# Optimization experiments

Measured on AMD Instinct MI355X. Metric: run time of the kernel, lower is better.

The kernel has to match this reference:

```python
import math
import jax, jax.numpy as jnp
import numpy as np

N = 8192
D_IN = 512
D_E = 512


def setup_inputs() -> dict:
    key = jax.random.key(0)
    k1, k2, k3, k4 = jax.random.split(key, 4)
    x = jax.random.normal(k1, (N, D_IN), dtype=jnp.float32)
    A = jax.random.uniform(k2, (N, N), dtype=jnp.float32)
    # xavier-uniform-ish scaling for the two projection weights
    lim_qkv = math.sqrt(6.0 / (D_IN + 3 * D_E))
    Wqkv = jax.random.uniform(k3, (D_IN, 3 * D_E), dtype=jnp.float32, minval=-lim_qkv, maxval=lim_qkv)
    bqkv = jnp.zeros((3 * D_E,), dtype=jnp.float32)
    lim_o = math.sqrt(6.0 / (D_E + D_E))
    Wo = jax.random.uniform(k4, (D_E, D_E), dtype=jnp.float32, minval=-lim_o, maxval=lim_o)
    bo = jnp.zeros((D_E,), dtype=jnp.float32)
    return {"x": x, "A": A, "Wqkv": Wqkv, "bqkv": bqkv, "Wo": Wo, "bo": bo}


def reference(x, A, Wqkv, bqkv, Wo, bo):
    # qkv projection: [N, 3*D_E]
    qkv = x @ Wqkv + bqkv
    q, k, v = jnp.split(qkv, 3, axis=-1)  # each [N, D_E]
    # graph-adjacency transform of keys
    k = A @ k  # [N, D_E]
    scale = 1.0 / math.sqrt(q.shape[-1])
    attn_logits = (q @ k.T) * scale  # [N, N]
    attention = jax.nn.softmax(attn_logits, axis=-1)
    values = attention @ v  # [N, D_E]
    o = values @ Wo + bo
    return (o, attention)
```

## Files before the change

### kernel.cpp

```cpp
#include <hip/hip_runtime.h>

typedef _Float16 half8 __attribute__((ext_vector_type(8)));
typedef _Float16 half4 __attribute__((ext_vector_type(4)));
typedef float f32x4 __attribute__((ext_vector_type(4)));

__global__ __launch_bounds__(256) void transpose_f32(
    const float* __restrict__ in, int lda,
    float* __restrict__ out, int ldo)
{
  __shared__ float t[32][33];
  const int tx = threadIdx.x & 31, ty = threadIdx.x >> 5;
  const int bc = blockIdx.x * 32, br = blockIdx.y * 32;
#pragma unroll
  for (int i = 0; i < 4; ++i)
    t[ty + 8 * i][tx] = in[(size_t)(br + ty + 8 * i) * lda + bc + tx];
  __syncthreads();
#pragma unroll
  for (int i = 0; i < 4; ++i)
    out[(size_t)(bc + ty + 8 * i) * ldo + br + tx] = t[tx][ty + 8 * i];
}

__global__ __launch_bounds__(256) void transpose_f32_f16(
    const float* __restrict__ in, int lda,
    _Float16* __restrict__ out, int ldo)
{
  __shared__ float t[32][33];
  const int tx = threadIdx.x & 31, ty = threadIdx.x >> 5;
  const int bc = blockIdx.x * 32, br = blockIdx.y * 32;
#pragma unroll
  for (int i = 0; i < 4; ++i)
    t[ty + 8 * i][tx] = in[(size_t)(br + ty + 8 * i) * lda + bc + tx];
  __syncthreads();
#pragma unroll
  for (int i = 0; i < 4; ++i)
    out[(size_t)(bc + ty + 8 * i) * ldo + br + tx] = (_Float16)t[tx][ty + 8 * i];
}

__global__ __launch_bounds__(256) void halfcolsum(
    const float* __restrict__ k0T, float* __restrict__ csum)
{
  const int d = blockIdx.x, tid = threadIdx.x;
  const float4* p = (const float4*)(k0T + (size_t)d * 8192);
  float s = 0.f;
#pragma unroll
  for (int i = 0; i < 8; ++i) {
    float4 v = p[i * 256 + tid];
    s += (v.x + v.y) + (v.z + v.w);
  }
#pragma unroll
  for (int off = 32; off; off >>= 1) s += __shfl_xor(s, off);
  __shared__ float r[4];
  if ((tid & 63) == 0) r[tid >> 6] = s;
  __syncthreads();
  if (tid == 0) csum[d] = 0.5f * ((r[0] + r[1]) + (r[2] + r[3]));
}

template<int ASPL,int BSPL,int BM,int BN,int WAVES_M,int WAVES_N,int THREADS,
         int APART,bool KSPLIT,bool QF16,int MINW>
__global__ __launch_bounds__(THREADS, MINW) void gemm_bt(
    const float* __restrict__ Ag, int lda, size_t a_plane,
    const float* __restrict__ Bg, int ldb,
    float* __restrict__ Cg, int ldc, size_t c_plane,
    const float* __restrict__ bias, int K, float scale,
    _Float16* __restrict__ q16out)
{
  constexpr int BK = 32;
  constexpr int WM = BM / WAVES_M, WN = BN / WAVES_N;
  constexpr int FM = WM / 16, FN = WN / 16;
  constexpr int NCA = (BM * 4) / THREADS;
  constexpr int NCB = (BN * 4) / THREADS;
  static_assert((BM * 4) % THREADS == 0 && (BN * 4) % THREADS == 0, "mismatch");

  __shared__ _Float16 ldsA[2][ASPL][BM][BK];
  __shared__ _Float16 ldsB[2][BSPL][BN][BK];

  const int tid  = threadIdx.x;
  const int lane = tid & 63;
  const int wid  = tid >> 6;
  const int wrow = wid / WAVES_N, wcol = wid % WAVES_N;
  const int l15  = lane & 15, g = lane >> 4;
  const int brow = blockIdx.y * BM;
  const int bcol = blockIdx.x * BN;

  if constexpr (KSPLIT) {
    const int kc = blockIdx.z;
    Ag += (size_t)kc * K;
    Bg += (size_t)kc * K;
    Cg += (size_t)kc * c_plane;
  }

  f32x4 acc[FM][FN];
#pragma unroll
  for (int mi = 0; mi < FM; ++mi)
#pragma unroll
    for (int ni = 0; ni < FN; ++ni)
      acc[mi][ni] = (f32x4){0.f, 0.f, 0.f, 0.f};

  float4 ra[NCA][2], rb[NCB][2];

  auto loadAB = [&](int kt) {
    const int k0 = kt * BK;
#pragma unroll
    for (int i = 0; i < NCA; ++i) {
      int c = tid + THREADS * i;
      int row = c >> 2, ci = c & 3;
      const float* bp = Ag + (size_t)(brow + row) * lda + k0 + ci * 8;
      float4 u0 = ((const float4*)bp)[0];
      float4 u1 = ((const float4*)bp)[1];
#pragma unroll
      for (int p = 1; p < APART; ++p) {
        const float* pp = bp + (size_t)p * a_plane;
        float4 w0 = ((const float4*)pp)[0], w1 = ((const float4*)pp)[1];
        u0.x += w0.x; u0.y += w0.y; u0.z += w0.z; u0.w += w0.w;
        u1.x += w1.x; u1.y += w1.y; u1.z += w1.z; u1.w += w1.w;
      }
      ra[i][0] = u0; ra[i][1] = u1;
    }
#pragma unroll
    for (int i = 0; i < NCB; ++i) {
      int c = tid + THREADS * i;
      int row = c >> 2, ci = c & 3;
      const float4* p = (const float4*)(Bg + (size_t)(bcol + row) * ldb + k0 + ci * 8);
      rb[i][0] = p[0]; rb[i][1] = p[1];
    }
  };

  auto stageLDS = [&](int b) {
#pragma unroll
    for (int i = 0; i < NCA; ++i) {
      int c = tid + THREADS * i;
      int row = c >> 2, ci = c & 3;
      float f[8] = {ra[i][0].x, ra[i][0].y, ra[i][0].z, ra[i][0].w,
                    ra[i][1].x, ra[i][1].y, ra[i][1].z, ra[i][1].w};
      half8 h, l;
#pragma unroll
      for (int j = 0; j < 8; ++j) {
        _Float16 hv = (_Float16)f[j];
        h[j] = hv;
        if (ASPL == 2) l[j] = (_Float16)(f[j] - (float)hv);
      }
      int off = row * BK + ((ci ^ ((row >> 1) & 3)) << 3);
      *(half8*)(&ldsA[b][0][0][0] + off) = h;
      if (ASPL == 2) *(half8*)(&ldsA[b][1][0][0] + off) = l;
    }
#pragma unroll
    for (int i = 0; i < NCB; ++i) {
      int c = tid + THREADS * i;
      int row = c >> 2, ci = c & 3;
      float f[8] = {rb[i][0].x, rb[i][0].y, rb[i][0].z, rb[i][0].w,
                    rb[i][1].x, rb[i][1].y, rb[i][1].z, rb[i][1].w};
      half8 h, l;
#pragma unroll
      for (int j = 0; j < 8; ++j) {
        _Float16 hv = (_Float16)f[j];
        h[j] = hv;
        if (BSPL == 2) l[j] = (_Float16)(f[j] - (float)hv);
      }
      int off = row * BK + ((ci ^ ((row >> 1) & 3)) << 3);
      *(half8*)(&ldsB[b][0][0][0] + off) = h;
      if (BSPL == 2) *(half8*)(&ldsB[b][1][0][0] + off) = l;
    }
  };

  const int nk = K / BK;
  loadAB(0);
  stageLDS(0);
  if (nk > 1) loadAB(1);
  __syncthreads();

  for (int kt = 0; kt < nk; ++kt) {
    const int cur = kt & 1, nxt = cur ^ 1;
    if (kt + 1 < nk) stageLDS(nxt);
    if (kt + 2 < nk) loadAB(kt + 2);

    half8 af[FM][ASPL];
#pragma unroll
    for (int mi = 0; mi < FM; ++mi)
#pragma unroll
      for (int sa = 0; sa < ASPL; ++sa) {
        int row = wrow * WM + mi * 16 + l15;
        af[mi][sa] = *(const half8*)(&ldsA[cur][sa][0][0] + row * BK + ((g ^ ((row >> 1) & 3)) << 3));
      }
#pragma unroll
    for (int ni = 0; ni < FN; ++ni) {
      half8 bf[BSPL];
#pragma unroll
      for (int sb = 0; sb < BSPL; ++sb) {
        int row = wcol * WN + ni * 16 + l15;
        bf[sb] = *(const half8*)(&ldsB[cur][sb][0][0] + row * BK + ((g ^ ((row >> 1) & 3)) << 3));
      }
#pragma unroll
      for (int mi = 0; mi < FM; ++mi)
#pragma unroll
        for (int sa = 0; sa < ASPL; ++sa)
#pragma unroll
          for (int sb = 0; sb < BSPL; ++sb) {
            if (ASPL == 2 && BSPL == 2 && sa == 1 && sb == 1) continue;
            acc[mi][ni] = __builtin_amdgcn_mfma_f32_16x16x32_f16(af[mi][sa], bf[sb], acc[mi][ni], 0, 0, 0);
          }
    }
    __syncthreads();
  }

#pragma unroll
  for (int mi = 0; mi < FM; ++mi)
#pragma unroll
    for (int ni = 0; ni < FN; ++ni) {
      int col = bcol + wcol * WN + ni * 16 + l15;
      float bv = bias ? bias[col] : 0.f;
#pragma unroll
      for (int j = 0; j < 4; ++j) {
        int r = brow + wrow * WM + mi * 16 + g * 4 + j;
        float v = acc[mi][ni][j] * scale + bv;
        Cg[(size_t)r * ldc + col] = v;
        if constexpr (QF16) {
          if (col < 512) q16out[(size_t)r * 512 + col] = (_Float16)v;
        }
      }
    }
}

template<int BM,int BN,int THREADS,bool STATS,int MINW>
__global__ __launch_bounds__(THREADS, MINW) void gemm_ff16(
    const _Float16* __restrict__ Ag, int lda,
    const _Float16* __restrict__ Bg, int ldb,
    float* __restrict__ Cg, int ldc,
    int K, float scale,
    float* __restrict__ mxout, float* __restrict__ smout, int ntiles)
{
  constexpr int BK = 32;
  constexpr int WAVES_M = 2, WAVES_N = 2;
  constexpr int WM = BM / WAVES_M, WN = BN / WAVES_N;
  constexpr int FM = WM / 16, FN = WN / 16;
  constexpr int NCA = (BM * 4) / THREADS;
  constexpr int NCB = (BN * 4) / THREADS;

  __shared__ _Float16 ldsA[2][BM][BK];
  __shared__ _Float16 ldsB[2][BN][BK];

  const int tid  = threadIdx.x;
  const int lane = tid & 63;
  const int wid  = tid >> 6;
  const int wrow = wid >> 1, wcol = wid & 1;
  const int l15  = lane & 15, g = lane >> 4;
  const int brow = blockIdx.y * BM;
  const int bcol = blockIdx.x * BN;

  f32x4 acc[FM][FN];
#pragma unroll
  for (int mi = 0; mi < FM; ++mi)
#pragma unroll
    for (int ni = 0; ni < FN; ++ni)
      acc[mi][ni] = (f32x4){0.f, 0.f, 0.f, 0.f};

  half8 ra[NCA], rb[NCB];

  auto loadAB = [&](int kt) {
    const int k0 = kt * BK;
#pragma unroll
    for (int i = 0; i < NCA; ++i) {
      int c = tid + THREADS * i;
      int row = c >> 2, ci = c & 3;
      ra[i] = *(const half8*)(Ag + (size_t)(brow + row) * lda + k0 + ci * 8);
    }
#pragma unroll
    for (int i = 0; i < NCB; ++i) {
      int c = tid + THREADS * i;
      int row = c >> 2, ci = c & 3;
      rb[i] = *(const half8*)(Bg + (size_t)(bcol + row) * ldb + k0 + ci * 8);
    }
  };

  auto stageLDS = [&](int b) {
#pragma unroll
    for (int i = 0; i < NCA; ++i) {
      int c = tid + THREADS * i;
      int row = c >> 2, ci = c & 3;
      int off = row * BK + ((ci ^ ((row >> 1) & 3)) << 3);
      *(half8*)(&ldsA[b][0][0] + off) = ra[i];
    }
#pragma unroll
    for (int i = 0; i < NCB; ++i) {
      int c = tid + THREADS * i;
      int row = c >> 2, ci = c & 3;
      int off = row * BK + ((ci ^ ((row >> 1) & 3)) << 3);
      *(half8*)(&ldsB[b][0][0] + off) = rb[i];
    }
  };

  const int nk = K / BK;
  loadAB(0);
  stageLDS(0);
  if (nk > 1) loadAB(1);
  __syncthreads();

  for (int kt = 0; kt < nk; ++kt) {
    const int cur = kt & 1, nxt = cur ^ 1;
    if (kt + 1 < nk) stageLDS(nxt);
    if (kt + 2 < nk) loadAB(kt + 2);

    half8 af[FM];
#pragma unroll
    for (int mi = 0; mi < FM; ++mi) {
      int row = wrow * WM + mi * 16 + l15;
      af[mi] = *(const half8*)(&ldsA[cur][0][0] + row * BK + ((g ^ ((row >> 1) & 3)) << 3));
    }
#pragma unroll
    for (int ni = 0; ni < FN; ++ni) {
      int row = wcol * WN + ni * 16 + l15;
      half8 bf = *(const half8*)(&ldsB[cur][0][0] + row * BK + ((g ^ ((row >> 1) & 3)) << 3));
#pragma unroll
      for (int mi = 0; mi < FM; ++mi)
        acc[mi][ni] = __builtin_amdgcn_mfma_f32_16x16x32_f16(af[mi], bf, acc[mi][ni], 0, 0, 0);
    }
    __syncthreads();
  }

#pragma unroll
  for (int mi = 0; mi < FM; ++mi)
#pragma unroll
    for (int ni = 0; ni < FN; ++ni) {
      int col = bcol + wcol * WN + ni * 16 + l15;
#pragma unroll
      for (int j = 0; j < 4; ++j) {
        int r = brow + wrow * WM + mi * 16 + g * 4 + j;
        Cg[(size_t)r * ldc + col] = acc[mi][ni][j] * scale;
      }
    }

  if constexpr (STATS) {
    __shared__ float s_m2[BM][2];
    __shared__ float s_s2[BM][2];
#pragma unroll
    for (int mi = 0; mi < FM; ++mi)
#pragma unroll
      for (int j = 0; j < 4; ++j) {
        float v = -3.4e38f;
#pragma unroll
        for (int ni = 0; ni < FN; ++ni) v = fmaxf(v, acc[mi][ni][j] * scale);
        v = fmaxf(v, __shfl_xor(v, 1)); v = fmaxf(v, __shfl_xor(v, 2));
        v = fmaxf(v, __shfl_xor(v, 4)); v = fmaxf(v, __shfl_xor(v, 8));
        if (l15 == 0) s_m2[wrow * WM + mi * 16 + g * 4 + j][wcol] = v;
      }
    __syncthreads();
#pragma unroll
    for (int mi = 0; mi < FM; ++mi)
#pragma unroll
      for (int j = 0; j < 4; ++j) {
        int r = wrow * WM + mi * 16 + g * 4 + j;
        float mt = fmaxf(s_m2[r][0], s_m2[r][1]);
        float s = 0.f;
#pragma unroll
        for (int ni = 0; ni < FN; ++ni) s += __expf(acc[mi][ni][j] * scale - mt);
        s += __shfl_xor(s, 1); s += __shfl_xor(s, 2);
        s += __shfl_xor(s, 4); s += __shfl_xor(s, 8);
        if (l15 == 0) s_s2[r][wcol] = s;
      }
    __syncthreads();
    if (tid < BM) {
      float mt = fmaxf(s_m2[tid][0], s_m2[tid][1]);
      float st = s_s2[tid][0] + s_s2[tid][1];
      mxout[(size_t)(brow + tid) * ntiles + blockIdx.x] = mt;
      smout[(size_t)(brow + tid) * ntiles + blockIdx.x] = st;
    }
  }
}

__global__ __launch_bounds__(256) void reduce4_f16(
    const float4* __restrict__ in, _Float16* __restrict__ out16, size_t plane4,
    const float4* __restrict__ csum4)
{
  size_t i = (size_t)blockIdx.x * 256 + threadIdx.x;
  float4 a = in[i], b = in[plane4 + i], c = in[2 * plane4 + i], d = in[3 * plane4 + i];
  float4 s = csum4[i & 127];
  half4 h;
  h[0] = (_Float16)(a.x + b.x + c.x + d.x - s.x);
  h[1] = (_Float16)(a.y + b.y + c.y + d.y - s.y);
  h[2] = (_Float16)(a.z + b.z + c.z + d.z - s.z);
  h[3] = (_Float16)(a.w + b.w + c.w + d.w - s.w);
  *(half4*)(out16 + i * 4) = h;
}

__global__ __launch_bounds__(256) void softmax_combine(
    const float* __restrict__ mx, const float* __restrict__ sm,
    float* __restrict__ rowm, float* __restrict__ rowinv)
{
  const int row = blockIdx.x * 4 + (threadIdx.x >> 6);
  const int lane = threadIdx.x & 63;
  float mt = mx[(size_t)row * 64 + lane];
  float m = mt;
#pragma unroll
  for (int off = 32; off; off >>= 1) m = fmaxf(m, __shfl_xor(m, off));
  float s = sm[(size_t)row * 64 + lane] * __expf(mt - m);
#pragma unroll
  for (int off = 32; off; off >>= 1) s += __shfl_xor(s, off);
  if (lane == 0) { rowm[row] = m; rowinv[row] = 1.0f / s; }
}

__global__ __launch_bounds__(512, 4) void pv_fused(
    float* __restrict__ attn,
    const _Float16* __restrict__ vT16,
    const float* __restrict__ rowm, const float* __restrict__ rowinv,
    float* __restrict__ vals_p)
{
  constexpr int BM = 64, BN = 512, BK = 32, NSTEP = 64;
  __shared__ _Float16 ldsA[2][BM][BK];
  __shared__ _Float16 ldsB[2][BN][BK];
  __shared__ float s_m[BM], s_inv[BM];

  const int tid = threadIdx.x, lane = tid & 63, wid = tid >> 6;
  const int wrow = wid >> 2, wcol = wid & 3;
  const int l15 = lane & 15, g = lane >> 4;
  const int kc = blockIdx.x, brow = blockIdx.y * BM;
  const size_t kbase = (size_t)kc * 2048;

  if (tid < BM) { s_m[tid] = rowm[brow + tid]; s_inv[tid] = rowinv[brow + tid]; }

  f32x4 acc[2][8];
#pragma unroll
  for (int mi = 0; mi < 2; ++mi)
#pragma unroll
    for (int ni = 0; ni < 8; ++ni) acc[mi][ni] = (f32x4){0.f, 0.f, 0.f, 0.f};

  const int arow = (tid & 255) >> 2, aci = tid & 3;
  float4 ra[2];
  half8 rbh[4];

  auto loadA = [&](int kt) {
    if (tid < 256) {
      const float4* p = (const float4*)(attn + (size_t)(brow + arow) * 8192 + kbase + kt * BK + aci * 8);
      ra[0] = p[0]; ra[1] = p[1];
    }
  };
  auto loadB = [&](int kt) {
#pragma unroll
    for (int i = 0; i < 4; ++i) {
      int c = tid + 512 * i; int r = c >> 2, ci = c & 3;
      rbh[i] = *(const half8*)(vT16 + (size_t)r * 8192 + kbase + kt * BK + ci * 8);
    }
  };
  auto stage = [&](int kt, int b) {
    if (tid < 256) {
      const float m = s_m[arow], inv = s_inv[arow];
      float f[8] = {ra[0].x, ra[0].y, ra[0].z, ra[0].w, ra[1].x, ra[1].y, ra[1].z, ra[1].w};
      float e[8]; half8 h;
#pragma unroll
      for (int j = 0; j < 8; ++j) {
        e[j] = __expf(f[j] - m) * inv;
        h[j] = (_Float16)e[j];
      }
      float4* w = (float4*)(attn + (size_t)(brow + arow) * 8192 + kbase + kt * BK + aci * 8);
      w[0] = make_float4(e[0], e[1], e[2], e[3]);
      w[1] = make_float4(e[4], e[5], e[6], e[7]);
      int off = arow * BK + ((aci ^ ((arow >> 1) & 3)) << 3);
      *(half8*)(&ldsA[b][0][0] + off) = h;
    }
#pragma unroll
    for (int i = 0; i < 4; ++i) {
      int c = tid + 512 * i; int r = c >> 2, ci = c & 3;
      int off2 = r * BK + ((ci ^ ((r >> 1) & 3)) << 3);
      *(half8*)(&ldsB[b][0][0] + off2) = rbh[i];
    }
  };

  loadA(0); loadB(0);
  __syncthreads();
  stage(0, 0);
  loadA(1); loadB(1);
  __syncthreads();

  for (int kt = 0; kt < NSTEP; ++kt) {
    const int cur = kt & 1, nxt = cur ^ 1;
    if (kt + 1 < NSTEP) stage(kt + 1, nxt);
    if (kt + 2 < NSTEP) { loadA(kt + 2); loadB(kt + 2); }
    half8 af[2];
#pragma unroll
    for (int mi = 0; mi < 2; ++mi) {
      int row = wrow * 32 + mi * 16 + l15;
      af[mi] = *(const half8*)(&ldsA[cur][0][0] + row * BK + ((g ^ ((row >> 1) & 3)) << 3));
    }
#pragma unroll
    for (int ni = 0; ni < 8; ++ni) {
      int rn = wcol * 128 + ni * 16 + l15;
      half8 bf = *(const half8*)(&ldsB[cur][0][0] + rn * BK + ((g ^ ((rn >> 1) & 3)) << 3));
#pragma unroll
      for (int mi = 0; mi < 2; ++mi)
        acc[mi][ni] = __builtin_amdgcn_mfma_f32_16x16x32_f16(af[mi], bf, acc[mi][ni], 0, 0, 0);
    }
    __syncthreads();
  }

  const size_t plane = (size_t)8192 * 512;
#pragma unroll
  for (int mi = 0; mi < 2; ++mi)
#pragma unroll
    for (int ni = 0; ni < 8; ++ni) {
      int col = wcol * 128 + ni * 16 + l15;
#pragma unroll
      for (int j = 0; j < 4; ++j) {
        int row = brow + wrow * 32 + mi * 16 + g * 4 + j;
        vals_p[(size_t)kc * plane + (size_t)row * 512 + col] = acc[mi][ni][j];
      }
    }
}

extern "C" void kernel_launch(void* const* d_in, const int* in_sizes, int n_in,
                              void* d_out, int out_size, void* d_ws, size_t ws_size,
                              hipStream_t stream)
{
  const float* x    = (const float*)d_in[0];
  const float* Amat = (const float*)d_in[1];
  const float* Wqkv = (const float*)d_in[2];
  const float* bqkv = (const float*)d_in[3];
  const float* Wo   = (const float*)d_in[4];
  const float* bo   = (const float*)d_in[5];

  float* o    = (float*)d_out;
  float* attn = (float*)d_out + (size_t)8192 * 512;

  float* ws = (float*)d_ws;
  float*     vals_p = ws;
  float*     qkv    = ws;
  float*     k0T    = ws + 12582912;
  _Float16*  vT16   = (_Float16*)(ws + 16777216);
  float*     WqkvT  = ws + 18874368;
  float*     WoT    = ws + 19660800;
  _Float16*  kbuf16 = (_Float16*)(ws + 19922944);
  float*     mx     = ws + 24117248;
  float*     sm     = ws + 24641536;
  float*     rowm   = ws + 25165824;
  float*     rowinv = ws + 25174016;
  float*     csum   = ws + 25182208;
  _Float16*  q16    = (_Float16*)(ws + 25183232);
  float*     kpart  = attn;

  const dim3 b256(256), b512(512);
  const float qk_scale = 0.04419417382415922f;
  const size_t plane = (size_t)8192 * 512;

  transpose_f32<<<dim3(48, 16), b256, 0, stream>>>(Wqkv, 1536, WqkvT, 512);
  transpose_f32<<<dim3(16, 16), b256, 0, stream>>>(Wo, 512, WoT, 512);

  gemm_bt<2, 2, 128, 128, 2, 2, 256, 1, false, true, 2>
      <<<dim3(12, 64), b256, 0, stream>>>(
      x, 512, 0, WqkvT, 512, qkv, 1536, 0, bqkv, 512, 1.0f, q16);

  transpose_f32<<<dim3(16, 256), b256, 0, stream>>>(qkv + 512, 1536, k0T, 8192);
  transpose_f32_f16<<<dim3(16, 256), b256, 0, stream>>>(qkv + 1024, 1536, vT16, 8192);
  halfcolsum<<<dim3(512), b256, 0, stream>>>(k0T, csum);

  gemm_bt<1, 2, 128, 256, 2, 4, 512, 1, true, false, 4>
      <<<dim3(2, 64, 4), b512, 0, stream>>>(
      Amat, 8192, 0, k0T, 8192, kpart, 512, plane, nullptr, 2048, 1.0f, nullptr);

  reduce4_f16<<<dim3(4096), b256, 0, stream>>>((const float4*)kpart, kbuf16, plane / 4,
                                               (const float4*)csum);

  gemm_ff16<128, 128, 256, true, 4>
      <<<dim3(64, 64), b256, 0, stream>>>(
      q16, 512, kbuf16, 512, attn, 8192, 512, qk_scale, mx, sm, 64);

  softmax_combine<<<dim3(2048), b256, 0, stream>>>(mx, sm, rowm, rowinv);

  pv_fused<<<dim3(4, 128), b512, 0, stream>>>(attn, vT16, rowm, rowinv, vals_p);

  gemm_bt<1, 1, 128, 128, 2, 2, 256, 4, false, false, 3>
      <<<dim3(4, 64), b256, 0, stream>>>(
      vals_p, 512, plane, WoT, 512, o, 512, 0, bo, 512, 1.0f, nullptr);
}
```

Measured before the change: 652.1 us.

## Load V fragments directly from global memory in pv_fused, dropping LDS staging

Removes the shared-memory staging buffer for the transposed V operand in the fused softmax-PV kernel. Each wave now owns a 64-column slice and reads its MFMA B fragments straight from global memory, changing the warp tiling from 2x8 to 4x4 per wave over all 64 rows. This cuts LDS traffic and capacity, which may allow more blocks per CU, but the B loads are now issued at the top of each step without prefetch, so global latency may be exposed.

```diff
diff --git a/kernel.cpp b/kernel.cpp
--- a/kernel.cpp
+++ b/kernel.cpp
@@ -403,40 +403,32 @@
     const float* __restrict__ rowm, const float* __restrict__ rowinv,
     float* __restrict__ vals_p)
 {
-  constexpr int BM = 64, BN = 512, BK = 32, NSTEP = 64;
+  constexpr int BM = 64, BK = 32, NSTEP = 64;
   __shared__ _Float16 ldsA[2][BM][BK];
-  __shared__ _Float16 ldsB[2][BN][BK];
   __shared__ float s_m[BM], s_inv[BM];
 
   const int tid = threadIdx.x, lane = tid & 63, wid = tid >> 6;
-  const int wrow = wid >> 2, wcol = wid & 3;
   const int l15 = lane & 15, g = lane >> 4;
   const int kc = blockIdx.x, brow = blockIdx.y * BM;
   const size_t kbase = (size_t)kc * 2048;
 
   if (tid < BM) { s_m[tid] = rowm[brow + tid]; s_inv[tid] = rowinv[brow + tid]; }
 
-  f32x4 acc[2][8];
-#pragma unroll
-  for (int mi = 0; mi < 2; ++mi)
-#pragma unroll
-    for (int ni = 0; ni < 8; ++ni) acc[mi][ni] = (f32x4){0.f, 0.f, 0.f, 0.f};
+  f32x4 acc[4][4];
+#pragma unroll
+  for (int mi = 0; mi < 4; ++mi)
+#pragma unroll
+    for (int ni = 0; ni < 4; ++ni) acc[mi][ni] = (f32x4){0.f, 0.f, 0.f, 0.f};
 
   const int arow = (tid & 255) >> 2, aci = tid & 3;
   float4 ra[2];
-  half8 rbh[4];
+
+  const _Float16* bbase = vT16 + (size_t)(wid * 64 + l15) * 8192 + kbase + g * 8;
 
   auto loadA = [&](int kt) {
     if (tid < 256) {
       const float4* p = (const float4*)(attn + (size_t)(brow + arow) * 8192 + kbase + kt * BK + aci * 8);
       ra[0] = p[0]; ra[1] = p[1];
-    }
-  };
-  auto loadB = [&](int kt) {
-#pragma unroll
-    for (int i = 0; i < 4; ++i) {
-      int c = tid + 512 * i; int r = c >> 2, ci = c & 3;
-      rbh[i] = *(const half8*)(vT16 + (size_t)r * 8192 + kbase + kt * BK + ci * 8);
     }
   };
   auto stage = [&](int kt, int b) {
@@ -455,50 +447,48 @@
       int off = arow * BK + ((aci ^ ((arow >> 1) & 3)) << 3);
       *(half8*)(&ldsA[b][0][0] + off) = h;
     }
-#pragma unroll
-    for (int i = 0; i < 4; ++i) {
-      int c = tid + 512 * i; int r = c >> 2, ci = c & 3;
-      int off2 = r * BK + ((ci ^ ((r >> 1) & 3)) << 3);
-      *(half8*)(&ldsB[b][0][0] + off2) = rbh[i];
-    }
   };
 
-  loadA(0); loadB(0);
+  loadA(0);
   __syncthreads();
   stage(0, 0);
-  loadA(1); loadB(1);
+  loadA(1);
   __syncthreads();
 
   for (int kt = 0; kt < NSTEP; ++kt) {
     const int cur = kt & 1, nxt = cur ^ 1;
+
+    half8 bf[4];
+#pragma unroll
+    for (int ni = 0; ni < 4; ++ni)
+      bf[ni] = *(const half8*)(bbase + (size_t)(ni * 16) * 8192 + kt * BK);
+
     if (kt + 1 < NSTEP) stage(kt + 1, nxt);
-    if (kt + 2 < NSTEP) { loadA(kt + 2); loadB(kt + 2); }
-    half8 af[2];
-#pragma unroll
-    for (int mi = 0; mi < 2; ++mi) {
-      int row = wrow * 32 + mi * 16 + l15;
+    if (kt + 2 < NSTEP) loadA(kt + 2);
+
+    half8 af[4];
+#pragma unroll
+    for (int mi = 0; mi < 4; ++mi) {
+      int row = mi * 16 + l15;
       af[mi] = *(const half8*)(&ldsA[cur][0][0] + row * BK + ((g ^ ((row >> 1) & 3)) << 3));
     }
 #pragma unroll
-    for (int ni = 0; ni < 8; ++ni) {
-      int rn = wcol * 128 + ni * 16 + l15;
-      half8 bf = *(const half8*)(&ldsB[cur][0][0] + rn * BK + ((g ^ ((rn >> 1) & 3)) << 3));
-#pragma unroll
-      for (int mi = 0; mi < 2; ++mi)
-        acc[mi][ni] = __builtin_amdgcn_mfma_f32_16x16x32_f16(af[mi], bf, acc[mi][ni], 0, 0, 0);
-    }
+    for (int ni = 0; ni < 4; ++ni)
+#pragma unroll
+      for (int mi = 0; mi < 4; ++mi)
+        acc[mi][ni] = __builtin_amdgcn_mfma_f32_16x16x32_f16(af[mi], bf[ni], acc[mi][ni], 0, 0, 0);
     __syncthreads();
   }
 
   const size_t plane = (size_t)8192 * 512;
 #pragma unroll
-  for (int mi = 0; mi < 2; ++mi)
-#pragma unroll
-    for (int ni = 0; ni < 8; ++ni) {
-      int col = wcol * 128 + ni * 16 + l15;
+  for (int mi = 0; mi < 4; ++mi)
+#pragma unroll
+    for (int ni = 0; ni < 4; ++ni) {
+      int col = wid * 64 + ni * 16 + l15;
 #pragma unroll
       for (int j = 0; j < 4; ++j) {
-        int row = brow + wrow * 32 + mi * 16 + g * 4 + j;
+        int row = brow + mi * 16 + g * 4 + j;
         vals_p[(size_t)kc * plane + (size_t)row * 512 + col] = acc[mi][ni][j];
       }
     }
```

Result: slower. 687.0 us (+5.4%).

## Remap A@K grid for XCD locality and restructure pv_fused pipeline

Applied to the files above, without the earlier changes.

The split-K A@K GEMM now launches a flat 1D grid whose block index is remapped so that blocks sharing the same A row tile and K chunk land on the same XCD. The goal is better L2 reuse of the large adjacency matrix. pv_fused now spreads the softmax-exp staging of the attention tile across all 512 threads instead of 256, with float4 chunks. It also unrolls the main loop by two with explicit double register buffers, prefetching two steps ahead, and raises wave priority around the MFMA block. These changes aim to cut load imbalance and stalls in the staging path, at the cost of more registers.

```diff
diff --git a/kernel.cpp b/kernel.cpp
--- a/kernel.cpp
+++ b/kernel.cpp
@@ -56,7 +56,7 @@
 }
 
 template<int ASPL,int BSPL,int BM,int BN,int WAVES_M,int WAVES_N,int THREADS,
-         int APART,bool KSPLIT,bool QF16,int MINW>
+         int APART,bool KSPLIT,bool QF16,int MINW,int SWZ>
 __global__ __launch_bounds__(THREADS, MINW) void gemm_bt(
     const float* __restrict__ Ag, int lda, size_t a_plane,
     const float* __restrict__ Bg, int ldb,
@@ -79,14 +79,25 @@
   const int wid  = tid >> 6;
   const int wrow = wid / WAVES_N, wcol = wid % WAVES_N;
   const int l15  = lane & 15, g = lane >> 4;
-  const int brow = blockIdx.y * BM;
-  const int bcol = blockIdx.x * BN;
+
+  int bx, by, bz;
+  if constexpr (SWZ == 1) {
+    const int id = blockIdx.x;
+    const int xcd = id & 7, s = id >> 3;
+    bx = s & 1;
+    const int p = (s >> 1) * 8 + xcd;
+    by = p & 63; bz = p >> 6;
+  } else {
+    bx = blockIdx.x; by = blockIdx.y; bz = blockIdx.z;
+  }
+
+  const int brow = by * BM;
+  const int bcol = bx * BN;
 
   if constexpr (KSPLIT) {
-    const int kc = blockIdx.z;
-    Ag += (size_t)kc * K;
-    Bg += (size_t)kc * K;
-    Cg += (size_t)kc * c_plane;
+    Ag += (size_t)bz * K;
+    Bg += (size_t)bz * K;
+    Cg += (size_t)bz * c_plane;
   }
 
   f32x4 acc[FM][FN];
@@ -403,9 +414,9 @@
     const float* __restrict__ rowm, const float* __restrict__ rowinv,
     float* __restrict__ vals_p)
 {
-  constexpr int BM = 64, BN = 512, BK = 32, NSTEP = 64;
+  constexpr int BM = 64, BK = 32, NSTEP = 64;
   __shared__ _Float16 ldsA[2][BM][BK];
-  __shared__ _Float16 ldsB[2][BN][BK];
+  __shared__ _Float16 ldsB[2][512][BK];
   __shared__ float s_m[BM], s_inv[BM];
 
   const int tid = threadIdx.x, lane = tid & 63, wid = tid >> 6;
@@ -422,71 +433,73 @@
 #pragma unroll
     for (int ni = 0; ni < 8; ++ni) acc[mi][ni] = (f32x4){0.f, 0.f, 0.f, 0.f};
 
-  const int arow = (tid & 255) >> 2, aci = tid & 3;
-  float4 ra[2];
-  half8 rbh[4];
-
-  auto loadA = [&](int kt) {
-    if (tid < 256) {
-      const float4* p = (const float4*)(attn + (size_t)(brow + arow) * 8192 + kbase + kt * BK + aci * 8);
-      ra[0] = p[0]; ra[1] = p[1];
-    }
-  };
-  auto loadB = [&](int kt) {
+  const int arow = tid >> 3, aci = tid & 7;
+
+  float4 ra0, ra1;
+  half8 rb0[4], rb1[4];
+
+  auto loadA = [&](int kt, float4& ra) {
+    ra = *(const float4*)(attn + (size_t)(brow + arow) * 8192 + kbase + kt * BK + aci * 4);
+  };
+  auto loadB = [&](int kt, half8* rb) {
 #pragma unroll
     for (int i = 0; i < 4; ++i) {
       int c = tid + 512 * i; int r = c >> 2, ci = c & 3;
-      rbh[i] = *(const half8*)(vT16 + (size_t)r * 8192 + kbase + kt * BK + ci * 8);
-    }
-  };
-  auto stage = [&](int kt, int b) {
-    if (tid < 256) {
-      const float m = s_m[arow], inv = s_inv[arow];
-      float f[8] = {ra[0].x, ra[0].y, ra[0].z, ra[0].w, ra[1].x, ra[1].y, ra[1].z, ra[1].w};
-      float e[8]; half8 h;
-#pragma unroll
-      for (int j = 0; j < 8; ++j) {
-        e[j] = __expf(f[j] - m) * inv;
-        h[j] = (_Float16)e[j];
-      }
-      float4* w = (float4*)(attn + (size_t)(brow + arow) * 8192 + kbase + kt * BK + aci * 8);
-      w[0] = make_float4(e[0], e[1], e[2], e[3]);
-      w[1] = make_float4(e[4], e[5], e[6], e[7]);
-      int off = arow * BK + ((aci ^ ((arow >> 1) & 3)) << 3);
-      *(half8*)(&ldsA[b][0][0] + off) = h;
-    }
+      rb[i] = *(const half8*)(vT16 + (size_t)r * 8192 + kbase + kt * BK + ci * 8);
+    }
+  };
+  auto stage = [&](int kt, int b, const float4& ra, const half8* rb) {
+    const float m = s_m[arow], inv = s_inv[arow];
+    float e0 = __expf(ra.x - m) * inv;
+    float e1 = __expf(ra.y - m) * inv;
+    float e2 = __expf(ra.z - m) * inv;
+    float e3 = __expf(ra.w - m) * inv;
+    *(float4*)(attn + (size_t)(brow + arow) * 8192 + kbase + kt * BK + aci * 4) =
+        make_float4(e0, e1, e2, e3);
+    half4 h; h[0] = (_Float16)e0; h[1] = (_Float16)e1; h[2] = (_Float16)e2; h[3] = (_Float16)e3;
+    int off = arow * BK + (((aci >> 1) ^ ((arow >> 1) & 3)) << 3) + ((aci & 1) << 2);
+    *(half4*)(&ldsA[b][0][0] + off) = h;
 #pragma unroll
     for (int i = 0; i < 4; ++i) {
       int c = tid + 512 * i; int r = c >> 2, ci = c & 3;
       int off2 = r * BK + ((ci ^ ((r >> 1) & 3)) << 3);
-      *(half8*)(&ldsB[b][0][0] + off2) = rbh[i];
-    }
-  };
-
-  loadA(0); loadB(0);
-  __syncthreads();
-  stage(0, 0);
-  loadA(1); loadB(1);
-  __syncthreads();
-
-  for (int kt = 0; kt < NSTEP; ++kt) {
-    const int cur = kt & 1, nxt = cur ^ 1;
-    if (kt + 1 < NSTEP) stage(kt + 1, nxt);
-    if (kt + 2 < NSTEP) { loadA(kt + 2); loadB(kt + 2); }
+      *(half8*)(&ldsB[b][0][0] + off2) = rb[i];
+    }
+  };
+  auto mfma_step = [&](int b) {
     half8 af[2];
 #pragma unroll
     for (int mi = 0; mi < 2; ++mi) {
       int row = wrow * 32 + mi * 16 + l15;
-      af[mi] = *(const half8*)(&ldsA[cur][0][0] + row * BK + ((g ^ ((row >> 1) & 3)) << 3));
-    }
+      af[mi] = *(const half8*)(&ldsA[b][0][0] + row * BK + ((g ^ ((row >> 1) & 3)) << 3));
+    }
+    __builtin_amdgcn_s_setprio(1);
 #pragma unroll
     for (int ni = 0; ni < 8; ++ni) {
       int rn = wcol * 128 + ni * 16 + l15;
-      half8 bf = *(const half8*)(&ldsB[cur][0][0] + rn * BK + ((g ^ ((rn >> 1) & 3)) << 3));
+      half8 bf = *(const half8*)(&ldsB[b][0][0] + rn * BK + ((g ^ ((rn >> 1) & 3)) << 3));
 #pragma unroll
       for (int mi = 0; mi < 2; ++mi)
         acc[mi][ni] = __builtin_amdgcn_mfma_f32_16x16x32_f16(af[mi], bf, acc[mi][ni], 0, 0, 0);
     }
+    __builtin_amdgcn_s_setprio(0);
+  };
+
+  loadA(0, ra0); loadB(0, rb0);
+  loadA(1, ra1); loadB(1, rb1);
+  __syncthreads();
+  stage(0, 0, ra0, rb0);
+  loadA(2, ra0); loadB(2, rb0);
+  __syncthreads();
+
+  for (int kt = 0; kt < NSTEP; kt += 2) {
+    if (kt + 1 < NSTEP) stage(kt + 1, 1, ra1, rb1);
+    if (kt + 3 < NSTEP) { loadA(kt + 3, ra1); loadB(kt + 3, rb1); }
+    mfma_step(0);
+    __syncthreads();
+    if (kt + 2 < NSTEP) stage(kt + 2, 0, ra0, rb0);
+    if (kt + 4 < NSTEP) { loadA(kt + 4, ra0); loadB(kt + 4, rb0); }
+    mfma_step(1);
     __syncthreads();
   }
 
@@ -541,7 +554,7 @@
   transpose_f32<<<dim3(48, 16), b256, 0, stream>>>(Wqkv, 1536, WqkvT, 512);
   transpose_f32<<<dim3(16, 16), b256, 0, stream>>>(Wo, 512, WoT, 512);
 
-  gemm_bt<2, 2, 128, 128, 2, 2, 256, 1, false, true, 2>
+  gemm_bt<2, 2, 128, 128, 2, 2, 256, 1, false, true, 2, 0>
       <<<dim3(12, 64), b256, 0, stream>>>(
       x, 512, 0, WqkvT, 512, qkv, 1536, 0, bqkv, 512, 1.0f, q16);
 
@@ -549,8 +562,8 @@
   transpose_f32_f16<<<dim3(16, 256), b256, 0, stream>>>(qkv + 1024, 1536, vT16, 8192);
   halfcolsum<<<dim3(512), b256, 0, stream>>>(k0T, csum);
 
-  gemm_bt<1, 2, 128, 256, 2, 4, 512, 1, true, false, 4>
-      <<<dim3(2, 64, 4), b512, 0, stream>>>(
+  gemm_bt<1, 2, 128, 256, 2, 4, 512, 1, true, false, 4, 1>
+      <<<dim3(512), b512, 0, stream>>>(
       Amat, 8192, 0, k0T, 8192, kpart, 512, plane, nullptr, 2048, 1.0f, nullptr);
 
   reduce4_f16<<<dim3(4096), b256, 0, stream>>>((const float4*)kpart, kbuf16, plane / 4,
@@ -564,7 +577,7 @@
 
   pv_fused<<<dim3(4, 128), b512, 0, stream>>>(attn, vT16, rowm, rowinv, vals_p);
 
-  gemm_bt<1, 1, 128, 128, 2, 2, 256, 4, false, false, 3>
+  gemm_bt<1, 1, 128, 128, 2, 2, 256, 4, false, false, 3, 0>
       <<<dim3(4, 64), b256, 0, stream>>>(
       vals_p, 512, plane, WoT, 512, o, 512, 0, bo, 512, 1.0f, nullptr);
 }
```

Result: slower. 778.6 us (+19.4%).
